# Optimization experiments

Measured on AMD Instinct MI355X. Metric: run time of the kernel, lower is better.

The kernel has to match this reference:

```python
import jax, jax.numpy as jnp
import numpy as np

# --- SLAYER SRM-alpha parameters (ncaltech101 yaml) ---
THETA = 10.0      # spike threshold
TAU_SR = 10.0     # synaptic response time constant
TAU_REF = 1.0     # refractory time constant
SCALE_REF = 2.0   # refractory scale
TAU_RHO = 1.0     # surrogate-pdf time constant
SCALE_RHO = 1.0   # surrogate-pdf scale
TS = 1.0          # simulation step
T_SAMPLE = 300    # number of time steps


def _alpha_kernel(tau, mult, Ts=TS, t_sample=T_SAMPLE):
    # SLAYER _calculateAlphaKernel: eps(t) = mult * t/tau * exp(1 - t/tau), truncated
    eps = []
    for t in np.arange(0.0, t_sample, Ts):
        v = mult * t / tau * np.exp(1.0 - t / tau)
        if abs(v) < 0.01 and t > tau:
            break
        eps.append(v)
    return np.asarray(eps, np.float32)

SRM_KERNEL = _alpha_kernel(TAU_SR, 1.0)                 # psp kernel, length ~76
REF_KERNEL = _alpha_kernel(TAU_REF, -SCALE_REF * THETA)  # refractory kernel, length ~12


def psp(x):
    """Causal temporal filter with the SRM alpha kernel. x: (B, N, T)."""
    eps = jnp.asarray(SRM_KERNEL)
    K = eps.shape[0]
    B, N, T = x.shape
    lhs = x.reshape(B * N, 1, T)
    rhs = eps[::-1].reshape(1, 1, K)  # flip: conv_general_dilated is correlation
    y = jax.lax.conv_general_dilated(lhs, rhs, window_strides=(1,),
                                     padding=[(K - 1, 0)],
                                     dimension_numbers=("NCH", "OIH", "NCH"))
    return y.reshape(B, N, T)


def _spike_scan(u):
    """Threshold + refractory reset over time. u: (B, N, T) -> (spikes, u_eff)."""
    ref = jnp.asarray(REF_KERNEL)  # (K,)
    B, N, T = u.shape
    K = ref.shape[0]

    def step(buf, u_t):
        # buf[..., 0] is the accumulated refractory contribution for this step
        u_eff = u_t + buf[..., 0]
        s = (u_eff >= THETA).astype(u_t.dtype)
        buf = buf + s[..., None] * ref            # add refractory kernel from new spikes
        buf = jnp.concatenate([buf[:, :, 1:], jnp.zeros_like(buf[:, :, :1])], axis=-1)
        return buf, (s, u_eff)

    buf0 = jnp.zeros((B, N, K), u.dtype)
    _, (s, u_eff) = jax.lax.scan(step, buf0, jnp.moveaxis(u, -1, 0))
    return jnp.moveaxis(s, 0, -1), jnp.moveaxis(u_eff, 0, -1)


@jax.custom_vjp
def spike(u):
    return _spike_scan(u)[0]


def _spike_fwd(u):
    s, u_eff = _spike_scan(u)
    return s, u_eff


def _spike_bwd(u_eff, g):
    # SLAYER surrogate gradient: scaleRho/(tauRho*theta) * exp(-|u - theta|/(tauRho*theta))
    tau = TAU_RHO * THETA
    pdf = (SCALE_RHO / tau) * jnp.exp(-jnp.abs(u_eff - THETA) / tau)
    return (g * pdf,)


spike.defvjp(_spike_fwd, _spike_bwd)


def setup_inputs() -> dict:
    key = jax.random.key(0)
    k1, k2, k3 = jax.random.split(key, 3)
    B, C, H, W, T = 2, 2, 200, 156, T_SAMPLE
    inp = (jax.random.uniform(k1, (B, C, H, W, T)) < 0.05).astype(jnp.float32)
    w1 = jax.random.normal(k2, (800, C * H * W), dtype=jnp.float32) * 0.05
    w2 = jax.random.normal(k3, (100, 800), dtype=jnp.float32) * 0.05
    return {"input": inp, "w1": w1, "w2": w2}


def reference(input, w1, w2):
    B, T = input.shape[0], input.shape[-1]
    x = input.reshape(B, -1, T)                      # (B, 62400, T)
    x = spike(psp(jnp.einsum("bft,of->bot", x, w1)))  # (B, 800, T)
    x = spike(psp(jnp.einsum("bft,of->bot", x, w2)))  # (B, 100, T)
    return x
```

## Files before the change

kernel.cpp:

```cpp
#include <hip/hip_runtime.h>

#define F1 62400
#define O1 800
#define O2N 100
#define TT 300
#define BB 2
#define NWRD 975
#define KSRM 77
#define KREF 11
#define M16 50
#define NPAD 640
#define NDIG 4
#define KSPL 10
#define WPS 98
#define BSTRIDE ((size_t)NPAD * 4)

#define NB_K1 2438

typedef unsigned long long u64;
typedef int i32x4 __attribute__((ext_vector_type(4)));

#define CSWZ(c) ((c) ^ ((((c) >> 4) & 3) << 1))

#define OFF_CONST 0ull
#define OFF_Z1P  1024ull
#define OFF_S1T  (OFF_Z1P + 40960000ull)
#define OFF_XBW  (OFF_S1T + 1920000ull)
#define OFF_Z1F  (OFF_XBW + 4992000ull)
#define OFF_U1   (OFF_Z1F + 3840000ull)
#define OFF_U2   (OFF_U1 + 3840000ull)
#define NEED_SPARSE (OFF_U2 + 480000ull)

__global__ void k0_init(double* c) {
    int k = threadIdx.x;
    if (k < KSRM) {
        double v = ((double)k / 10.0) * exp(1.0 - (double)k / 10.0);
        c[k] = (double)(float)v;
    }
    if (k < KREF) {
        double v = -20.0 * (double)k * exp(1.0 - (double)k);
        c[80 + k] = (double)(float)v;
    }
}

__global__ __launch_bounds__(256) void k_pre(const float* __restrict__ x,
                                             u64* __restrict__ xbw,
                                             double* __restrict__ cst) {
    int blk = blockIdx.x;
    if (blk < NB_K1) {
        const int NTG = 5;
        int gw = (blk * 256 + (int)threadIdx.x) >> 6;
        int lane = threadIdx.x & 63;
        if (gw >= BB * NWRD * NTG) return;
        int b  = gw / (NWRD * NTG);
        int r  = gw % (NWRD * NTG);
        int fw = r / NTG;
        int tg = r % NTG;
        int t = tg * 64 + lane;
        bool act = (t < TT);
        int tc = act ? t : 0;
        const float* xp = x + ((size_t)(b * F1 + (fw << 6))) * TT + tc;
        unsigned lo = 0, hi = 0;
        #pragma unroll
        for (int j = 0; j < 32; ++j)
            lo |= (xp[(size_t)j * TT] > 0.5f ? 1u : 0u) << j;
        #pragma unroll
        for (int j = 0; j < 32; ++j)
            hi |= (xp[(size_t)(j + 32) * TT] > 0.5f ? 1u : 0u) << j;
        u64 mval = act ? (((u64)hi << 32) | lo) : 0ull;
        xbw[(size_t)fw * NPAD + b * 320 + t] = mval;
    } else {
        int k = threadIdx.x;
        if (k < KSRM) {
            double v = ((double)k / 10.0) * exp(1.0 - (double)k / 10.0);
            cst[k] = (double)(float)v;
        }
        if (k < KREF) {
            double v = -20.0 * (double)k * exp(1.0 - (double)k);
            cst[80 + k] = (double)(float)v;
        }
    }
}

__device__ __forceinline__ void quant2(float2 f, unsigned short dg[4]) {
    int v0 = (int)rintf(f.x * 2147483648.0f);
    int v1 = (int)rintf(f.y * 2147483648.0f);
    int r0 = (v0 + 128) >> 8, s0 = (v1 + 128) >> 8;
    int r1 = (r0 + 128) >> 8, s1 = (s0 + 128) >> 8;
    int r2 = (r1 + 128) >> 8, s2 = (s1 + 128) >> 8;
    dg[0] = (unsigned short)((v0 & 0xFF) | ((v1 & 0xFF) << 8));
    dg[1] = (unsigned short)((r0 & 0xFF) | ((s0 & 0xFF) << 8));
    dg[2] = (unsigned short)((r1 & 0xFF) | ((s1 & 0xFF) << 8));
    dg[3] = (unsigned short)((r2 & 0xFF) | ((s2 & 0xFF) << 8));
}

#define K3_COMPUTE(A0, A1, A2, A3, BV, TTI)                                        \
    {                                                                              \
        i32x4 bf;                                                                  \
        _Pragma("unroll")                                                          \
        for (int i_ = 0; i_ < 4; ++i_)                                             \
            bf[i_] = (int)((((BV >> (4 * i_)) & 0xFu) * 0x00204081u) & 0x01010101u); \
        acc[TTI][0] = __builtin_amdgcn_mfma_i32_16x16x64_i8(A0, bf, acc[TTI][0], 0, 0, 0); \
        acc[TTI][1] = __builtin_amdgcn_mfma_i32_16x16x64_i8(A1, bf, acc[TTI][1], 0, 0, 0); \
        acc[TTI][2] = __builtin_amdgcn_mfma_i32_16x16x64_i8(A2, bf, acc[TTI][2], 0, 0, 0); \
        acc[TTI][3] = __builtin_amdgcn_mfma_i32_16x16x64_i8(A3, bf, acc[TTI][3], 0, 0, 0); \
    }

#define K_ITER(S, FQ, FI, BU0, BU1, BU2, BU3, BU4, BL0, BL1, BL2, BL3, BL4)        \
    {                                                                              \
        int s_ = (S);                                                              \
        if (s_ < steps) {                                                          \
            int pf = s_ + 2; if (pf > steps - 1) pf = steps - 1;                   \
            FI = *(const float2*)(fbase + (size_t)pf * 64);                        \
            int sn = s_ + 1; if (sn > steps - 1) sn = steps - 1;                   \
            const unsigned short* bpn = bp0 + (size_t)sn * BSTRIDE;                \
            BL0 = bpn[0]; BL1 = bpn[64]; BL2 = bpn[128]; BL3 = bpn[192]; BL4 = bpn[256]; \
            const char* lp = &Abuf[s_ & 1][0] + lofs;                              \
            i32x4 a0 = *(const i32x4*)(lp);                                        \
            i32x4 a1 = *(const i32x4*)(lp + 1024);                                 \
            i32x4 a2 = *(const i32x4*)(lp + 2048);                                 \
            i32x4 a3 = *(const i32x4*)(lp + 3072);                                 \
            K3_COMPUTE(a0, a1, a2, a3, BU0, 0)                                     \
            K3_COMPUTE(a0, a1, a2, a3, BU1, 1)                                     \
            K3_COMPUTE(a0, a1, a2, a3, BU2, 2)                                     \
            K3_COMPUTE(a0, a1, a2, a3, BU3, 3)                                     \
            K3_COMPUTE(a0, a1, a2, a3, BU4, 4)                                     \
            unsigned short dg[4];                                                  \
            quant2(FQ, dg);                                                        \
            char* wb = &Abuf[(s_ + 1) & 1][0] + wofs;                              \
            *(unsigned short*)(wb)        = dg[0];                                 \
            *(unsigned short*)(wb + 1024) = dg[1];                                 \
            *(unsigned short*)(wb + 2048) = dg[2];                                 \
            *(unsigned short*)(wb + 3072) = dg[3];                                 \
        }                                                                          \
        __syncthreads();                                                           \
    }

__global__ __launch_bounds__(512, 4) void k3m2(const float* __restrict__ w1,
                                               const u64* __restrict__ xbw,
                                               u64* __restrict__ z1p) {
    __shared__ __align__(16) char Abuf[2][4096];
    int m16 = blockIdx.x, ksl = blockIdx.y;
    int tid = threadIdx.x;
    int l = tid & 63, wid = tid >> 6;
    int o  = tid >> 5;
    int kp = tid & 31;

    int wl0 = ksl * WPS;
    int wend = wl0 + WPS; if (wend > NWRD) wend = NWRD;
    int steps = wend - wl0;

    i32x4 acc[5][NDIG];
    #pragma unroll
    for (int i = 0; i < 5; ++i)
        #pragma unroll
        for (int d = 0; d < NDIG; ++d) acc[i][d] = (i32x4){0, 0, 0, 0};

    const float* fbase = w1 + (size_t)(m16 * 16 + o) * F1 + (size_t)wl0 * 64 + kp * 2;
    const unsigned short* bp0 =
        (const unsigned short*)((const char*)xbw
            + ((size_t)wl0 * NPAD
               + (size_t)(wid * 80 + (l & 15))) * 8
            + (l >> 4) * 2);
    const int lofs = CSWZ(l) * 16;
    const int wc = (kp >> 3) * 16 + o;
    const int wofs = CSWZ(wc) * 16 + (kp & 7) * 2;

    float2 fA, fB, fC;
    unsigned bA0, bA1, bA2, bA3, bA4;
    unsigned bB0, bB1, bB2, bB3, bB4;
    unsigned bC0, bC1, bC2, bC3, bC4;

    fA = *(const float2*)(fbase);
    {
        unsigned short dg[4];
        quant2(fA, dg);
        char* wb = &Abuf[0][0] + wofs;
        *(unsigned short*)(wb)        = dg[0];
        *(unsigned short*)(wb + 1024) = dg[1];
        *(unsigned short*)(wb + 2048) = dg[2];
        *(unsigned short*)(wb + 3072) = dg[3];
    }
    fB = *(const float2*)(fbase + ((steps > 1) ? 64 : 0));
    bA0 = bp0[0]; bA1 = bp0[64]; bA2 = bp0[128]; bA3 = bp0[192]; bA4 = bp0[256];
    __syncthreads();

    int smax3 = ((steps + 2) / 3) * 3;
    #pragma unroll 1
    for (int sb = 0; sb < smax3; sb += 3) {
        K_ITER(sb,     fB, fC, bA0, bA1, bA2, bA3, bA4, bB0, bB1, bB2, bB3, bB4)
        K_ITER(sb + 1, fC, fA, bB0, bB1, bB2, bB3, bB4, bC0, bC1, bC2, bC3, bC4)
        K_ITER(sb + 2, fA, fB, bC0, bC1, bC2, bC3, bC4, bA0, bA1, bA2, bA3, bA4)
    }

    u64* zp = z1p + (size_t)ksl * O1 * NPAD;
    #pragma unroll
    for (int tt = 0; tt < 5; ++tt) {
        int n = wid * 80 + tt * 16 + (l & 15);
        #pragma unroll
        for (int r = 0; r < 4; ++r) {
            int oo = m16 * 16 + (l >> 4) * 4 + r;
            long long c = (long long)acc[tt][0][r]
                        + ((long long)acc[tt][1][r] << 8)
                        + ((long long)acc[tt][2][r] << 16)
                        + ((long long)acc[tt][3][r] << 24);
            zp[(size_t)oo * NPAD + n] = (u64)c;
        }
    }
}

__global__ __launch_bounds__(256) void k_dense_gemm1(const float* __restrict__ x,
                                                     const float* __restrict__ w1,
                                                     double* __restrict__ z1) {
    int lin = blockIdx.x;
    int ot = lin % 25; int tt = (lin / 25) % 5; int b = lin / 125;
    int t0 = tt * 64, o0 = ot * 32;
    __shared__ float xs[64][64];
    __shared__ float wsh[32][64];
    int ti = threadIdx.x & 63, og = threadIdx.x >> 6;
    double dacc[8] = {0, 0, 0, 0, 0, 0, 0, 0};
    for (int fc = 0; fc < F1; fc += 64) {
        __syncthreads();
        for (int e = threadIdx.x; e < 64 * 64; e += 256) {
            int r = e >> 6, c = e & 63;
            int t = t0 + c;
            xs[r][c] = (t < TT) ? x[((size_t)b * F1 + fc + r) * TT + t] : 0.0f;
        }
        for (int e = threadIdx.x; e < 32 * 64; e += 256) {
            int r = e >> 6, c = e & 63;
            wsh[r][c] = w1[(size_t)(o0 + r) * F1 + fc + c];
        }
        __syncthreads();
        float facc[8] = {0, 0, 0, 0, 0, 0, 0, 0};
        for (int ff = 0; ff < 64; ++ff) {
            float xv = xs[ff][ti];
            #pragma unroll
            for (int oo = 0; oo < 8; ++oo) facc[oo] += wsh[og * 8 + oo][ff] * xv;
        }
        #pragma unroll
        for (int oo = 0; oo < 8; ++oo) dacc[oo] += (double)facc[oo];
    }
    int t = t0 + ti;
    if (t < TT) {
        #pragma unroll
        for (int oo = 0; oo < 8; ++oo) {
            int o = o0 + og * 8 + oo;
            z1[((size_t)(b * O1 + o)) * TT + t] = dacc[oo];
        }
    }
}

__global__ __launch_bounds__(320) void k_conv1(const u64* __restrict__ z1p,
                                               const double* __restrict__ z1f,
                                               double* __restrict__ u1,
                                               const double* __restrict__ cst,
                                               int mode) {
    __shared__ double zs[TT];
    __shared__ double ck[KSRM];
    int row = blockIdx.x;
    int b = row / O1, o = row % O1;
    int t = threadIdx.x;
    if (t < KSRM) ck[t] = cst[t];
    if (t < TT) {
        double z;
        if (mode == 0) {
            long long c = 0;
            size_t base = (size_t)o * NPAD + b * 320 + t;
            #pragma unroll
            for (int g = 0; g < KSPL; ++g)
                c += (long long)z1p[(size_t)g * O1 * NPAD + base];
            z = (double)c * 4.656612873077393e-10;
        } else {
            z = z1f[(size_t)row * TT + t];
        }
        zs[t] = z;
    }
    __syncthreads();
    if (t < TT) {
        int kmax = t < (KSRM - 1) ? t : (KSRM - 1);
        double acc = 0.0;
        for (int k = 0; k <= kmax; ++k) acc += ck[k] * zs[t - k];
        u1[(size_t)row * TT + t] = acc;
    }
}

__global__ __launch_bounds__(64) void k_scan(const double* __restrict__ u,
                                             float* __restrict__ s,
                                             const double* __restrict__ cst,
                                             int nrows) {
    int row = blockIdx.x * 64 + threadIdx.x;
    if (row >= nrows) return;
    double rk1 = cst[81], rk2 = cst[82], rk3 = cst[83], rk4 = cst[84];
    double rk5 = cst[85], rk6 = cst[86], rk7 = cst[87], rk8 = cst[88];
    double rk9 = cst[89], rk10 = cst[90];
    const double* ur = u + (size_t)row * TT;
    float* sr = s + (size_t)row * TT;
    double buf[30];
    #pragma unroll
    for (int j = 0; j < 30; ++j) buf[j] = ur[j];
    unsigned h = 0;
    #pragma unroll 1
    for (int tb = 0; tb < TT; tb += 30) {
        double nxt[30];
        #pragma unroll
        for (int j = 0; j < 30; ++j) {
            int tn = tb + 30 + j; if (tn > TT - 1) tn = TT - 1;
            nxt[j] = ur[tn];
        }
        #pragma unroll
        for (int j = 0; j < 30; ++j) {
            double a  = ((h & 1u)   ? rk1 : 0.0) + ((h & 2u)   ? rk2  : 0.0);
            double b2 = ((h & 4u)   ? rk3 : 0.0) + ((h & 8u)   ? rk4  : 0.0);
            double c2 = ((h & 16u)  ? rk5 : 0.0) + ((h & 32u)  ? rk6  : 0.0);
            double d2 = ((h & 64u)  ? rk7 : 0.0) + ((h & 128u) ? rk8  : 0.0);
            double e2 = ((h & 256u) ? rk9 : 0.0) + ((h & 512u) ? rk10 : 0.0);
            double ueff = buf[j] + (((a + b2) + (c2 + d2)) + e2);
            unsigned sp = (ueff >= 10.0) ? 1u : 0u;
            sr[tb + j] = (float)sp;
            h = (h << 1) | sp;
        }
        #pragma unroll
        for (int j = 0; j < 30; ++j) buf[j] = nxt[j];
    }
}

__global__ __launch_bounds__(320) void k_gemm2c(const float* __restrict__ s1t,
                                                const float* __restrict__ w2,
                                                double* __restrict__ u2,
                                                const double* __restrict__ cst) {
    __shared__ float wsm[O1];
    __shared__ double zs[TT];
    __shared__ double ck[KSRM];
    int bo = blockIdx.x;
    int b = bo / O2N, o2 = bo % O2N;
    int t = threadIdx.x;
    if (t < KSRM) ck[t] = cst[t];
    for (int f = t; f < O1; f += 320) wsm[f] = w2[(size_t)o2 * O1 + f];
    __syncthreads();
    if (t < TT) {
        double acc = 0.0;
        #pragma unroll 4
        for (int f = 0; f < O1; ++f)
            acc += (double)(wsm[f] * s1t[((size_t)(b * O1 + f)) * TT + t]);
        zs[t] = acc;
    }
    __syncthreads();
    if (t < TT) {
        int kmax = t < (KSRM - 1) ? t : (KSRM - 1);
        double acc = 0.0;
        for (int k = 0; k <= kmax; ++k) acc += ck[k] * zs[t - k];
        u2[(size_t)bo * TT + t] = acc;
    }
}

extern "C" void kernel_launch(void* const* d_in, const int* in_sizes, int n_in,
                              void* d_out, int out_size, void* d_ws, size_t ws_size,
                              hipStream_t stream) {
    const float* x  = (const float*)d_in[0];
    const float* w1 = (const float*)d_in[1];
    const float* w2 = (const float*)d_in[2];
    float* out = (float*)d_out;
    char* ws = (char*)d_ws;

    double* cst = (double*)(ws + OFF_CONST);
    u64*    z1p = (u64*)   (ws + OFF_Z1P);
    float*  s1t = (float*) (ws + OFF_S1T);
    u64*    xbw = (u64*)   (ws + OFF_XBW);
    double* z1f = (double*)(ws + OFF_Z1F);
    double* u1  = (double*)(ws + OFF_U1);
    double* u2  = (double*)(ws + OFF_U2);

    int mode;
    if (ws_size >= NEED_SPARSE) {
        mode = 0;
        k_pre<<<NB_K1 + 1, 256, 0, stream>>>(x, xbw, cst);
        k3m2<<<dim3(M16, KSPL), 512, 0, stream>>>(w1, xbw, z1p);
    } else {
        mode = 1;
        k0_init<<<1, 128, 0, stream>>>(cst);
        k_dense_gemm1<<<250, 256, 0, stream>>>(x, w1, z1f);
    }

    k_conv1<<<BB * O1, 320, 0, stream>>>(z1p, z1f, u1, cst, mode);
    k_scan<<<(BB * O1 + 63) / 64, 64, 0, stream>>>(u1, s1t, cst, BB * O1);
    k_gemm2c<<<BB * O2N, 320, 0, stream>>>(s1t, w2, u2, cst);
    k_scan<<<(BB * O2N + 63) / 64, 64, 0, stream>>>(u2, out, cst, BB * O2N);
    (void)in_sizes; (void)n_in; (void)out_size;
}
```

Baseline: 282.1 us.

## Widen GEMM1 output tile from 16 to 32 rows per block

The int8-digit MFMA GEMM kernel now computes 32 output rows per block instead of 16. Each block reuses its bitpacked spike B-fragments across two A halves, and each thread loads float4 weights and packs four values into dword LDS stores. This halves the grid and the redundant xbw loads and unpacking per output. In exchange it doubles the accumulator registers (40 i32x4), doubles LDS, and lowers the occupancy target to 2 blocks per CU, leaving only 250 blocks.

```diff
diff --git a/kernel.cpp b/kernel.cpp
--- a/kernel.cpp
+++ b/kernel.cpp
@@ -8,7 +8,7 @@
 #define NWRD 975
 #define KSRM 77
 #define KREF 11
-#define M16 50
+#define M32 25
 #define NPAD 640
 #define NDIG 4
 #define KSPL 10
@@ -82,28 +82,34 @@
     }
 }
 
-__device__ __forceinline__ void quant2(float2 f, unsigned short dg[4]) {
-    int v0 = (int)rintf(f.x * 2147483648.0f);
-    int v1 = (int)rintf(f.y * 2147483648.0f);
-    int r0 = (v0 + 128) >> 8, s0 = (v1 + 128) >> 8;
-    int r1 = (r0 + 128) >> 8, s1 = (s0 + 128) >> 8;
-    int r2 = (r1 + 128) >> 8, s2 = (s1 + 128) >> 8;
-    dg[0] = (unsigned short)((v0 & 0xFF) | ((v1 & 0xFF) << 8));
-    dg[1] = (unsigned short)((r0 & 0xFF) | ((s0 & 0xFF) << 8));
-    dg[2] = (unsigned short)((r1 & 0xFF) | ((s1 & 0xFF) << 8));
-    dg[3] = (unsigned short)((r2 & 0xFF) | ((s2 & 0xFF) << 8));
-}
-
-#define K3_COMPUTE(A0, A1, A2, A3, BV, TTI)                                        \
+__device__ __forceinline__ void quant4(float4 f, unsigned dw[4]) {
+    float ff[4] = {f.x, f.y, f.z, f.w};
+    dw[0] = 0; dw[1] = 0; dw[2] = 0; dw[3] = 0;
+    #pragma unroll
+    for (int e = 0; e < 4; ++e) {
+        int v  = (int)rintf(ff[e] * 2147483648.0f);
+        int r0 = (v + 128) >> 8;
+        int r1 = (r0 + 128) >> 8;
+        int r2 = (r1 + 128) >> 8;
+        dw[0] |= (unsigned)(v  & 0xFF) << (8 * e);
+        dw[1] |= (unsigned)(r0 & 0xFF) << (8 * e);
+        dw[2] |= (unsigned)(r1 & 0xFF) << (8 * e);
+        dw[3] |= (unsigned)(r2 & 0xFF) << (8 * e);
+    }
+}
+
+#define K3_TILE(BV, TTI)                                                           \
     {                                                                              \
         i32x4 bf;                                                                  \
         _Pragma("unroll")                                                          \
         for (int i_ = 0; i_ < 4; ++i_)                                             \
             bf[i_] = (int)((((BV >> (4 * i_)) & 0xFu) * 0x00204081u) & 0x01010101u); \
-        acc[TTI][0] = __builtin_amdgcn_mfma_i32_16x16x64_i8(A0, bf, acc[TTI][0], 0, 0, 0); \
-        acc[TTI][1] = __builtin_amdgcn_mfma_i32_16x16x64_i8(A1, bf, acc[TTI][1], 0, 0, 0); \
-        acc[TTI][2] = __builtin_amdgcn_mfma_i32_16x16x64_i8(A2, bf, acc[TTI][2], 0, 0, 0); \
-        acc[TTI][3] = __builtin_amdgcn_mfma_i32_16x16x64_i8(A3, bf, acc[TTI][3], 0, 0, 0); \
+        _Pragma("unroll")                                                          \
+        for (int h_ = 0; h_ < 2; ++h_)                                             \
+            _Pragma("unroll")                                                      \
+            for (int d_ = 0; d_ < NDIG; ++d_)                                      \
+                acc[TTI][h_][d_] = __builtin_amdgcn_mfma_i32_16x16x64_i8(          \
+                    a[h_][d_], bf, acc[TTI][h_][d_], 0, 0, 0);                     \
     }
 
 #define K_ITER(S, FQ, FI, BU0, BU1, BU2, BU3, BU4, BL0, BL1, BL2, BL3, BL4)        \
@@ -111,77 +117,81 @@
         int s_ = (S);                                                              \
         if (s_ < steps) {                                                          \
             int pf = s_ + 2; if (pf > steps - 1) pf = steps - 1;                   \
-            FI = *(const float2*)(fbase + (size_t)pf * 64);                        \
+            FI = *(const float4*)(fbase + (size_t)pf * 64);                        \
             int sn = s_ + 1; if (sn > steps - 1) sn = steps - 1;                   \
             const unsigned short* bpn = bp0 + (size_t)sn * BSTRIDE;                \
             BL0 = bpn[0]; BL1 = bpn[64]; BL2 = bpn[128]; BL3 = bpn[192]; BL4 = bpn[256]; \
-            const char* lp = &Abuf[s_ & 1][0] + lofs;                              \
-            i32x4 a0 = *(const i32x4*)(lp);                                        \
-            i32x4 a1 = *(const i32x4*)(lp + 1024);                                 \
-            i32x4 a2 = *(const i32x4*)(lp + 2048);                                 \
-            i32x4 a3 = *(const i32x4*)(lp + 3072);                                 \
-            K3_COMPUTE(a0, a1, a2, a3, BU0, 0)                                     \
-            K3_COMPUTE(a0, a1, a2, a3, BU1, 1)                                     \
-            K3_COMPUTE(a0, a1, a2, a3, BU2, 2)                                     \
-            K3_COMPUTE(a0, a1, a2, a3, BU3, 3)                                     \
-            K3_COMPUTE(a0, a1, a2, a3, BU4, 4)                                     \
-            unsigned short dg[4];                                                  \
-            quant2(FQ, dg);                                                        \
+            const char* lp = &Abuf[s_ & 1][0];                                     \
+            i32x4 a[2][4];                                                         \
+            _Pragma("unroll")                                                      \
+            for (int h_ = 0; h_ < 2; ++h_)                                         \
+                _Pragma("unroll")                                                  \
+                for (int d_ = 0; d_ < NDIG; ++d_)                                  \
+                    a[h_][d_] = *(const i32x4*)(lp + h_ * 4096 + d_ * 1024 + lofs); \
+            K3_TILE(BU0, 0)                                                        \
+            K3_TILE(BU1, 1)                                                        \
+            K3_TILE(BU2, 2)                                                        \
+            K3_TILE(BU3, 3)                                                        \
+            K3_TILE(BU4, 4)                                                        \
+            unsigned dwq[4];                                                       \
+            quant4(FQ, dwq);                                                       \
             char* wb = &Abuf[(s_ + 1) & 1][0] + wofs;                              \
-            *(unsigned short*)(wb)        = dg[0];                                 \
-            *(unsigned short*)(wb + 1024) = dg[1];                                 \
-            *(unsigned short*)(wb + 2048) = dg[2];                                 \
-            *(unsigned short*)(wb + 3072) = dg[3];                                 \
+            *(unsigned*)(wb)        = dwq[0];                                      \
+            *(unsigned*)(wb + 1024) = dwq[1];                                      \
+            *(unsigned*)(wb + 2048) = dwq[2];                                      \
+            *(unsigned*)(wb + 3072) = dwq[3];                                      \
         }                                                                          \
         __syncthreads();                                                           \
     }
 
-__global__ __launch_bounds__(512, 4) void k3m2(const float* __restrict__ w1,
+__global__ __launch_bounds__(512, 2) void k3m2(const float* __restrict__ w1,
                                                const u64* __restrict__ xbw,
                                                u64* __restrict__ z1p) {
-    __shared__ __align__(16) char Abuf[2][4096];
-    int m16 = blockIdx.x, ksl = blockIdx.y;
+    __shared__ __align__(16) char Abuf[2][8192];
+    int m32 = blockIdx.x, ksl = blockIdx.y;
     int tid = threadIdx.x;
     int l = tid & 63, wid = tid >> 6;
-    int o  = tid >> 5;
-    int kp = tid & 31;
+    int o  = tid >> 4;
+    int kq = tid & 15;
 
     int wl0 = ksl * WPS;
     int wend = wl0 + WPS; if (wend > NWRD) wend = NWRD;
     int steps = wend - wl0;
 
-    i32x4 acc[5][NDIG];
+    i32x4 acc[5][2][NDIG];
     #pragma unroll
     for (int i = 0; i < 5; ++i)
         #pragma unroll
-        for (int d = 0; d < NDIG; ++d) acc[i][d] = (i32x4){0, 0, 0, 0};
-
-    const float* fbase = w1 + (size_t)(m16 * 16 + o) * F1 + (size_t)wl0 * 64 + kp * 2;
+        for (int h = 0; h < 2; ++h)
+            #pragma unroll
+            for (int d = 0; d < NDIG; ++d) acc[i][h][d] = (i32x4){0, 0, 0, 0};
+
+    const float* fbase = w1 + (size_t)(m32 * 32 + o) * F1 + (size_t)wl0 * 64 + kq * 4;
     const unsigned short* bp0 =
         (const unsigned short*)((const char*)xbw
             + ((size_t)wl0 * NPAD
                + (size_t)(wid * 80 + (l & 15))) * 8
             + (l >> 4) * 2);
     const int lofs = CSWZ(l) * 16;
-    const int wc = (kp >> 3) * 16 + o;
-    const int wofs = CSWZ(wc) * 16 + (kp & 7) * 2;
-
-    float2 fA, fB, fC;
+    const int wc = (kq >> 2) * 16 + (o & 15);
+    const int wofs = (o >> 4) * 4096 + CSWZ(wc) * 16 + (kq & 3) * 4;
+
+    float4 fA, fB, fC;
     unsigned bA0, bA1, bA2, bA3, bA4;
     unsigned bB0, bB1, bB2, bB3, bB4;
     unsigned bC0, bC1, bC2, bC3, bC4;
 
-    fA = *(const float2*)(fbase);
+    fA = *(const float4*)(fbase);
     {
-        unsigned short dg[4];
-        quant2(fA, dg);
+        unsigned dwq[4];
+        quant4(fA, dwq);
         char* wb = &Abuf[0][0] + wofs;
-        *(unsigned short*)(wb)        = dg[0];
-        *(unsigned short*)(wb + 1024) = dg[1];
-        *(unsigned short*)(wb + 2048) = dg[2];
-        *(unsigned short*)(wb + 3072) = dg[3];
-    }
-    fB = *(const float2*)(fbase + ((steps > 1) ? 64 : 0));
+        *(unsigned*)(wb)        = dwq[0];
+        *(unsigned*)(wb + 1024) = dwq[1];
+        *(unsigned*)(wb + 2048) = dwq[2];
+        *(unsigned*)(wb + 3072) = dwq[3];
+    }
+    fB = *(const float4*)(fbase + ((steps > 1) ? 64 : 0));
     bA0 = bp0[0]; bA1 = bp0[64]; bA2 = bp0[128]; bA3 = bp0[192]; bA4 = bp0[256];
     __syncthreads();
 
@@ -198,13 +208,16 @@
     for (int tt = 0; tt < 5; ++tt) {
         int n = wid * 80 + tt * 16 + (l & 15);
         #pragma unroll
-        for (int r = 0; r < 4; ++r) {
-            int oo = m16 * 16 + (l >> 4) * 4 + r;
-            long long c = (long long)acc[tt][0][r]
-                        + ((long long)acc[tt][1][r] << 8)
-                        + ((long long)acc[tt][2][r] << 16)
-                        + ((long long)acc[tt][3][r] << 24);
-            zp[(size_t)oo * NPAD + n] = (u64)c;
+        for (int h = 0; h < 2; ++h) {
+            #pragma unroll
+            for (int r = 0; r < 4; ++r) {
+                int oo = m32 * 32 + h * 16 + (l >> 4) * 4 + r;
+                long long c = (long long)acc[tt][h][0][r]
+                            + ((long long)acc[tt][h][1][r] << 8)
+                            + ((long long)acc[tt][h][2][r] << 16)
+                            + ((long long)acc[tt][h][3][r] << 24);
+                zp[(size_t)oo * NPAD + n] = (u64)c;
+            }
         }
     }
 }
@@ -374,7 +387,7 @@
     if (ws_size >= NEED_SPARSE) {
         mode = 0;
         k_pre<<<NB_K1 + 1, 256, 0, stream>>>(x, xbw, cst);
-        k3m2<<<dim3(M16, KSPL), 512, 0, stream>>>(w1, xbw, z1p);
+        k3m2<<<dim3(M32, KSPL), 512, 0, stream>>>(w1, xbw, z1p);
     } else {
         mode = 1;
         k0_init<<<1, 128, 0, stream>>>(cst);
```

Result: faster. 270.3 us (-4.2%).
